# Kernel optimization log

Hardware: AMD Instinct MI355X
Metric: run time of the kernel (lower is better)

Reference implementation:

```python
import jax, jax.numpy as jnp
import numpy as np

N_EMBD = 768
N_HEAD = 12
HEAD_DIM = N_EMBD // N_HEAD
B, S = 2, 2048


def setup_inputs() -> dict:
    key = jax.random.key(0)
    k1, k2, k3 = jax.random.split(key, 3)
    scale = 0.02
    return {
        "hidden_states": jax.random.normal(k1, (B, S, N_EMBD), dtype=jnp.float32),
        "w_attn": jax.random.normal(k2, (N_EMBD, 3 * N_EMBD), dtype=jnp.float32) * scale,
        "b_attn": jnp.zeros((3 * N_EMBD,), dtype=jnp.float32),
        "w_proj": jax.random.normal(k3, (N_EMBD, N_EMBD), dtype=jnp.float32) * scale,
        "b_proj": jnp.zeros((N_EMBD,), dtype=jnp.float32),
    }


def reference(hidden_states, w_attn, b_attn, w_proj, b_proj):
    b, s, d = hidden_states.shape
    qkv = hidden_states @ w_attn + b_attn  # [B,S,3D]
    q, k, v = jnp.split(qkv, 3, axis=-1)
    # split heads: [B,S,D] -> [B,H,S,hd]
    def split_heads(t):
        return t.reshape(b, s, N_HEAD, HEAD_DIM).transpose(0, 2, 1, 3)
    q, k, v = split_heads(q), split_heads(k), split_heads(v)
    scores = jnp.einsum("bhqd,bhkd->bhqk", q, k) / jnp.sqrt(jnp.float32(HEAD_DIM))
    # causal mask: strict upper triangle -> -inf
    mask = jnp.triu(jnp.ones((s, s), dtype=bool), k=1)
    scores = jnp.where(mask, -jnp.inf, scores)
    attn = jax.nn.softmax(scores, axis=-1)
    out = jnp.einsum("bhqk,bhkd->bhqd", attn, v)  # [B,H,S,hd]
    out = out.transpose(0, 2, 1, 3).reshape(b, s, d)  # merge heads
    return out @ w_proj + b_proj
```

## Files before the change

### kernel.cpp

```cpp
#include <hip/hip_runtime.h>
#include <hip/hip_bf16.h>

#define BATCH 2
#define SEQ   2048
#define DMODEL 768
#define NHEAD 12
#define HDIM  64
#define QKVD  2304

typedef __bf16 bf16x8 __attribute__((ext_vector_type(8)));
typedef float f32x4 __attribute__((ext_vector_type(4)));
typedef float f32x16 __attribute__((ext_vector_type(16)));

static __device__ inline f32x4 mfma16(bf16x8 a, bf16x8 b, f32x4 c) {
    return __builtin_amdgcn_mfma_f32_16x16x32_bf16(a, b, c, 0, 0, 0);
}
static __device__ inline f32x16 mfma32(bf16x8 a, bf16x8 b, f32x16 c) {
    return __builtin_amdgcn_mfma_f32_32x32x16_bf16(a, b, c, 0, 0, 0);
}

static __device__ inline unsigned short f2bf_bits(float f) {
    __hip_bfloat16 h = __float2bfloat16(f);
    return __builtin_bit_cast(unsigned short, h);
}
static __device__ inline unsigned int pack_bf16(float a, float b) {
    return (unsigned int)f2bf_bits(a) | ((unsigned int)f2bf_bits(b) << 16);
}

static __device__ inline void gload16(const __hip_bfloat16* g, __hip_bfloat16* l) {
    __builtin_amdgcn_global_load_lds(
        (const __attribute__((address_space(1))) void*)g,
        (__attribute__((address_space(3))) void*)l, 16, 0, 0);
}


__global__ __launch_bounds__(256) void f32_to_bf16_k(const float* __restrict__ in,
                                                     __hip_bfloat16* __restrict__ out) {
    int i = blockIdx.x * 256 + threadIdx.x;
    float4 v = reinterpret_cast<const float4*>(in)[i];
    ushort4 o;
    o.x = f2bf_bits(v.x); o.y = f2bf_bits(v.y);
    o.z = f2bf_bits(v.z); o.w = f2bf_bits(v.w);
    reinterpret_cast<ushort4*>(out)[i] = o;
}

__global__ __launch_bounds__(256) void transpose_f32_to_bf16(const float* __restrict__ in,
                                                             __hip_bfloat16* __restrict__ out,
                                                             int R, int C) {
    __shared__ float t[32][33];
    int tx = threadIdx.x & 31, ty = threadIdx.x >> 5;
    int bx = blockIdx.x * 32;
    int by = blockIdx.y * 32;
#pragma unroll
    for (int k = 0; k < 4; k++)
        t[ty + k * 8][tx] = in[(size_t)(by + ty + k * 8) * C + bx + tx];
    __syncthreads();
#pragma unroll
    for (int k = 0; k < 4; k++)
        out[(size_t)(bx + ty + k * 8) * R + by + tx] = __float2bfloat16(t[tx][ty + k * 8]);
}


__global__ __launch_bounds__(256) void pack_kv(const __hip_bfloat16* __restrict__ qkv,
                                               __hip_bfloat16* __restrict__ Kp,
                                               __hip_bfloat16* __restrict__ Vp) {
    __shared__ __hip_bfloat16 Kl[32][72];
    __shared__ __hip_bfloat16 Vl[32][72];
    int tid = threadIdx.x;
    int q32 = blockIdx.x;
    int bh = blockIdx.y;
    int b = bh / NHEAD, h = bh - (bh / NHEAD) * NHEAD;
    int row = tid >> 3, cc = (tid & 7) * 8;
    const __hip_bfloat16* src = qkv + (size_t)(b * SEQ + q32 * 32 + row) * QKVD + h * HDIM + cc;
    *reinterpret_cast<uint4*>(&Kl[row][cc]) = *reinterpret_cast<const uint4*>(src + DMODEL);
    *reinterpret_cast<uint4*>(&Vl[row][cc]) = *reinterpret_cast<const uint4*>(src + 2 * DMODEL);
    __syncthreads();

    int l31 = tid & 31, half = (tid >> 5) & 1;
    size_t obase = (size_t)bh * 131072 + (size_t)q32 * 2048 + (size_t)tid * 8;

    int kd = tid >> 6;
    bf16x8 kf = *reinterpret_cast<const bf16x8*>(&Kl[l31][kd * 16 + half * 8]);
    *reinterpret_cast<bf16x8*>(Kp + obase) = kf;

    int ks = tid >> 7, dh = (tid >> 6) & 1;
    union { unsigned short s[8]; bf16x8 v; } vf;
#pragma unroll
    for (int i = 0; i < 8; i++)
        vf.s[i] = __builtin_bit_cast(unsigned short, Vl[ks * 16 + half * 8 + i][dh * 32 + l31]);
    *reinterpret_cast<bf16x8*>(Vp + obase) = vf.v;
}


template <bool OUT_BF16>
__global__ __launch_bounds__(256) void gemm_bt(const __hip_bfloat16* __restrict__ A,
                                               const __hip_bfloat16* __restrict__ Bt,
                                               const float* __restrict__ bias,
                                               void* __restrict__ Cp,
                                               int M, int N, int K, int lda) {
    __shared__ __hip_bfloat16 Al[2][128 * 32];
    __shared__ __hip_bfloat16 Bl[2][128 * 32];

    int tid = threadIdx.x;
    int wid = tid >> 6;
    int lane = tid & 63;
    int lr = lane & 15;
    int lg = lane >> 4;
    int m0 = blockIdx.y * 128;
    int n0 = blockIdx.x * 128;
    int wm = (wid >> 1) * 64;
    int wn = (wid & 1) * 64;

    int srow = wid * 16 + (lane >> 2);
    int scol = (lane & 3) * 8;
    const __hip_bfloat16* ag = A + (size_t)(m0 + srow) * lda + scol;
    const __hip_bfloat16* bg = Bt + (size_t)(n0 + srow) * K + scol;
    int lofs = wid * 512;

    f32x4 acc[4][4] = {};

    gload16(ag, &Al[0][lofs]);
    gload16(ag + (size_t)64 * lda, &Al[0][lofs + 2048]);
    gload16(bg, &Bl[0][lofs]);
    gload16(bg + (size_t)64 * K, &Bl[0][lofs + 2048]);
    __syncthreads();

    int nk = K >> 5;
    for (int t = 0; t < nk; t++) {
        int cb = t & 1;
        if (t + 1 < nk) {
            int k0 = (t + 1) << 5;
            int nb = cb ^ 1;
            gload16(ag + k0, &Al[nb][lofs]);
            gload16(ag + (size_t)64 * lda + k0, &Al[nb][lofs + 2048]);
            gload16(bg + k0, &Bl[nb][lofs]);
            gload16(bg + (size_t)64 * K + k0, &Bl[nb][lofs + 2048]);
        }

        bf16x8 af[4], bfr[4];
#pragma unroll
        for (int i = 0; i < 4; i++)
            af[i] = *reinterpret_cast<const bf16x8*>(&Al[cb][(wm + i * 16 + lr) * 32 + lg * 8]);
#pragma unroll
        for (int j = 0; j < 4; j++)
            bfr[j] = *reinterpret_cast<const bf16x8*>(&Bl[cb][(wn + j * 16 + lr) * 32 + lg * 8]);
#pragma unroll
        for (int i = 0; i < 4; i++)
#pragma unroll
            for (int j = 0; j < 4; j++)
                acc[i][j] = mfma16(af[i], bfr[j], acc[i][j]);
        __syncthreads();
    }

#pragma unroll
    for (int i = 0; i < 4; i++) {
#pragma unroll
        for (int j = 0; j < 4; j++) {
            int col = n0 + wn + j * 16 + lr;
            float bv = bias[col];
#pragma unroll
            for (int r = 0; r < 4; r++) {
                int row = m0 + wm + i * 16 + lg * 4 + r;
                float v = acc[i][j][r] + bv;
                if (OUT_BF16)
                    ((__hip_bfloat16*)Cp)[(size_t)row * N + col] = __float2bfloat16(v);
                else
                    ((float*)Cp)[(size_t)row * N + col] = v;
            }
        }
    }
}


#define KS2 0.18033688f

__global__ __launch_bounds__(256, 4) void flash_attn(const __hip_bfloat16* __restrict__ qkv,
                                                     const __hip_bfloat16* __restrict__ Kp,
                                                     const __hip_bfloat16* __restrict__ Vp,
                                                     __hip_bfloat16* __restrict__ obase) {
    __shared__ __align__(16) char smem[30208];

    int tid = threadIdx.x;
    int w = tid >> 6;
    int lane = tid & 63;
    int l31 = lane & 31;
    int lg2 = lane >> 5;

    int wg = blockIdx.x;
    int xcd = wg & 7;
    int slot = wg >> 3;
    int hsl = slot % 3;
    int qsl = slot / 3;
    int bh = xcd * 3 + hsl;
    int it = 63 - qsl;
    int b = bh / NHEAD;
    int h = bh - b * NHEAD;
    int q0 = it * 32;
    int bbase = b * SEQ;

    int Tw = (it >= w) ? ((it - w) >> 2) + 1 : 0;

    const __hip_bfloat16* Kph = Kp + (size_t)bh * 131072;
    const __hip_bfloat16* Vph = Vp + (size_t)bh * 131072;

    const __hip_bfloat16* qg = qkv + (size_t)(bbase + q0 + l31) * QKVD + h * HDIM;
    bf16x8 qf[4];
#pragma unroll
    for (int kd = 0; kd < 4; kd++)
        qf[kd] = *reinterpret_cast<const bf16x8*>(qg + kd * 16 + lg2 * 8);

    f32x16 o0 = {}, o1 = {};
    float m = -3.0e38f, l = 0.f;

    bf16x8 kc[4];
    {
        const __hip_bfloat16* kr = Kph + (size_t)w * 2048 + l31 * 8;
#pragma unroll
        for (int kd = 0; kd < 4; kd++)
            kc[kd] = *reinterpret_cast<const bf16x8*>(kr + (kd * 2 + lg2) * 256);
    }

    for (int t = 0; t < Tw; t++) {
        int qi = 4 * t + w;
        int kvbase = qi * 32;
        bool hn = (t + 1 < Tw);

        const __hip_bfloat16* vr = Vph + (size_t)qi * 2048 + lg2 * 256 + l31 * 8;
        bf16x8 vf[4];
#pragma unroll
        for (int ks = 0; ks < 2; ks++)
#pragma unroll
            for (int dh = 0; dh < 2; dh++)
                vf[ks * 2 + dh] = *reinterpret_cast<const bf16x8*>(vr + (ks * 2 + dh) * 512);

        __builtin_amdgcn_s_setprio(1);
        f32x16 st = {};
#pragma unroll
        for (int kd = 0; kd < 4; kd++)
            st = mfma32(kc[kd], qf[kd], st);
        __builtin_amdgcn_s_setprio(0);

        if (hn) {
            const __hip_bfloat16* kr = Kph + (size_t)(qi + 4) * 2048 + l31 * 8;
#pragma unroll
            for (int kd = 0; kd < 4; kd++)
                kc[kd] = *reinterpret_cast<const bf16x8*>(kr + (kd * 2 + lg2) * 256);
        }

        if (kvbase == q0) {
#pragma unroll
            for (int j = 0; j < 16; j++) {
                int kvl = (j & 3) + 8 * (j >> 2) + 4 * lg2;
                if (kvl > l31) st[j] = -3.0e38f;
            }
        }
        float tm[16];
#pragma unroll
        for (int j = 0; j < 16; j++) tm[j] = st[j];
#pragma unroll
        for (int dd = 8; dd >= 1; dd >>= 1)
#pragma unroll
            for (int j = 0; j < 8; j++)
                if (j < dd) tm[j] = fmaxf(tm[j], tm[j + dd]);
        float mx = fmaxf(tm[0], __shfl_xor(tm[0], 32, 64));
        bool small = __all(mx <= m + 44.0f);
        float mnew = small ? m : fmaxf(m, mx);
#pragma unroll
        for (int j = 0; j < 16; j++)
            st[j] = __builtin_amdgcn_exp2f((st[j] - mnew) * KS2);
        float ts[16];
#pragma unroll
        for (int j = 0; j < 16; j++) ts[j] = st[j];
#pragma unroll
        for (int dd = 8; dd >= 1; dd >>= 1)
#pragma unroll
            for (int j = 0; j < 8; j++)
                if (j < dd) ts[j] += ts[j + dd];
        float ls = ts[0] + __shfl_xor(ts[0], 32, 64);
        if (small) {
            l += ls;
        } else {
            float sc = __builtin_amdgcn_exp2f((m - mnew) * KS2);
            l = l * sc + ls;
            o0 *= sc;
            o1 *= sc;
            m = mnew;
        }

#pragma unroll
        for (int ks = 0; ks < 2; ks++) {
            unsigned int a0 = pack_bf16(st[8 * ks + 0], st[8 * ks + 1]);
            unsigned int a1 = pack_bf16(st[8 * ks + 2], st[8 * ks + 3]);
            unsigned int b0 = pack_bf16(st[8 * ks + 4], st[8 * ks + 5]);
            unsigned int b1 = pack_bf16(st[8 * ks + 6], st[8 * ks + 7]);
            unsigned int y0 = lg2 ? a0 : b0;
            unsigned int y1 = lg2 ? a1 : b1;
            unsigned int p0 = __shfl_xor(y0, 32, 64);
            unsigned int p1 = __shfl_xor(y1, 32, 64);
            union { unsigned int u[4]; bf16x8 v; } pf;
            pf.u[0] = lg2 ? p0 : a0;
            pf.u[1] = lg2 ? p1 : a1;
            pf.u[2] = lg2 ? b0 : p0;
            pf.u[3] = lg2 ? b1 : p1;
            __builtin_amdgcn_s_setprio(1);
            o0 = mfma32(vf[ks * 2 + 0], pf.v, o0);
            o1 = mfma32(vf[ks * 2 + 1], pf.v, o1);
            __builtin_amdgcn_s_setprio(0);
        }
    }

    __syncthreads();

    if (w != 0) {
        float* SCw = (float*)(smem + (w - 1) * 8448);
#pragma unroll
        for (int j = 0; j < 16; j++) {
            int dl = (j & 3) + 8 * (j >> 2) + 4 * lg2;
            SCw[dl * 32 + l31] = o0[j];
            SCw[(32 + dl) * 32 + l31] = o1[j];
        }
        if (lg2 == 0) {
            SCw[2048 + l31] = m;
            SCw[2048 + 32 + l31] = l;
        }
    }
    __syncthreads();
    if (w == 0) {
        float* SC1 = (float*)(smem + 0);
        float* SC2 = (float*)(smem + 8448);
        float* SC3 = (float*)(smem + 16896);
        __hip_bfloat16* OL = (__hip_bfloat16*)(smem + 25344);
        float m1 = SC1[2048 + l31], l1 = SC1[2048 + 32 + l31];
        float m2 = SC2[2048 + l31], l2 = SC2[2048 + 32 + l31];
        float m3 = SC3[2048 + l31], l3 = SC3[2048 + 32 + l31];
        float M = fmaxf(fmaxf(m, m1), fmaxf(m2, m3));
        float e0 = __builtin_amdgcn_exp2f((m - M) * KS2);
        float e1 = __builtin_amdgcn_exp2f((m1 - M) * KS2);
        float e2 = __builtin_amdgcn_exp2f((m2 - M) * KS2);
        float e3 = __builtin_amdgcn_exp2f((m3 - M) * KS2);
        float L = l * e0 + l1 * e1 + l2 * e2 + l3 * e3;
        float linv = 1.0f / L;
#pragma unroll
        for (int od = 0; od < 2; od++) {
#pragma unroll
            for (int g = 0; g < 4; g++) {
                int dbase = od * 32 + 8 * g + 4 * lg2;
                ushort4 w4;
#pragma unroll
                for (int r = 0; r < 4; r++) {
                    int d = dbase + r;
                    float self = od ? o1[4 * g + r] : o0[4 * g + r];
                    float v = self * e0 + SC1[d * 32 + l31] * e1 +
                              SC2[d * 32 + l31] * e2 + SC3[d * 32 + l31] * e3;
                    v *= linv;
                    ((unsigned short*)&w4)[r] = f2bf_bits(v);
                }
                *reinterpret_cast<ushort4*>(&OL[l31 * 72 + dbase]) = w4;
            }
        }
    }
    __syncthreads();
    {
        __hip_bfloat16* OL = (__hip_bfloat16*)(smem + 25344);
        int r = tid >> 3, c = (tid & 7) * 8;
        __hip_bfloat16* dst = obase + (size_t)(bbase + q0 + r) * QKVD + h * HDIM + c;
        *reinterpret_cast<uint4*>(dst) = *reinterpret_cast<const uint4*>(&OL[r * 72 + c]);
    }
}


extern "C" void kernel_launch(void* const* d_in, const int* in_sizes, int n_in,
                              void* d_out, int out_size, void* d_ws, size_t ws_size,
                              hipStream_t stream) {
    const float* hidden = (const float*)d_in[0];
    const float* w_attn = (const float*)d_in[1];
    const float* b_attn = (const float*)d_in[2];
    const float* w_proj = (const float*)d_in[3];
    const float* b_proj = (const float*)d_in[4];
    float* out = (float*)d_out;

    char* ws = (char*)d_ws;
    __hip_bfloat16* Xb  = (__hip_bfloat16*)(ws + 0);
    __hip_bfloat16* Wta = (__hip_bfloat16*)(ws + 6291456);
    __hip_bfloat16* Wtp = (__hip_bfloat16*)(ws + 9830400);
    __hip_bfloat16* QKV = (__hip_bfloat16*)(ws + 11010048);
    __hip_bfloat16* Kpb = (__hip_bfloat16*)(ws + 0);
    __hip_bfloat16* Vpb = (__hip_bfloat16*)(ws + 29884416);

    const int M = BATCH * SEQ;

    f32_to_bf16_k<<<dim3(M * DMODEL / (256 * 4)), dim3(256), 0, stream>>>(hidden, Xb);
    transpose_f32_to_bf16<<<dim3(QKVD / 32, DMODEL / 32), dim3(256), 0, stream>>>(w_attn, Wta, DMODEL, QKVD);
    transpose_f32_to_bf16<<<dim3(DMODEL / 32, DMODEL / 32), dim3(256), 0, stream>>>(w_proj, Wtp, DMODEL, DMODEL);
    gemm_bt<true><<<dim3(QKVD / 128, M / 128), dim3(256), 0, stream>>>(Xb, Wta, b_attn, QKV, M, QKVD, DMODEL, DMODEL);
    pack_kv<<<dim3(SEQ / 32, BATCH * NHEAD), dim3(256), 0, stream>>>(QKV, Kpb, Vpb);
    flash_attn<<<dim3(1536), dim3(256), 0, stream>>>(QKV, Kpb, Vpb, QKV + DMODEL);
    gemm_bt<false><<<dim3(DMODEL / 128, M / 128), dim3(256), 0, stream>>>(QKV + DMODEL, Wtp, b_proj, out, M, DMODEL, DMODEL, QKVD);
}
```

Baseline: 94.40 us.

## Fuse K/V packing into QKV GEMM epilogue and drop pack_kv kernel

```diff
diff --git a/kernel.cpp b/kernel.cpp
--- a/kernel.cpp
+++ b/kernel.cpp
@@ -61,34 +61,108 @@
 }
 
 
-__global__ __launch_bounds__(256) void pack_kv(const __hip_bfloat16* __restrict__ qkv,
-                                               __hip_bfloat16* __restrict__ Kp,
-                                               __hip_bfloat16* __restrict__ Vp) {
-    __shared__ __hip_bfloat16 Kl[32][72];
-    __shared__ __hip_bfloat16 Vl[32][72];
+__global__ __launch_bounds__(256) void gemm_qkv(const __hip_bfloat16* __restrict__ A,
+                                                const __hip_bfloat16* __restrict__ Bt,
+                                                const float* __restrict__ bias,
+                                                __hip_bfloat16* __restrict__ Qp,
+                                                __hip_bfloat16* __restrict__ Kp,
+                                                __hip_bfloat16* __restrict__ Vp,
+                                                int M, int N, int K) {
+    __shared__ __hip_bfloat16 Al[2][128 * 32];
+    __shared__ __hip_bfloat16 Bl[2][128 * 32];
+
     int tid = threadIdx.x;
-    int q32 = blockIdx.x;
-    int bh = blockIdx.y;
-    int b = bh / NHEAD, h = bh - (bh / NHEAD) * NHEAD;
-    int row = tid >> 3, cc = (tid & 7) * 8;
-    const __hip_bfloat16* src = qkv + (size_t)(b * SEQ + q32 * 32 + row) * QKVD + h * HDIM + cc;
-    *reinterpret_cast<uint4*>(&Kl[row][cc]) = *reinterpret_cast<const uint4*>(src + DMODEL);
-    *reinterpret_cast<uint4*>(&Vl[row][cc]) = *reinterpret_cast<const uint4*>(src + 2 * DMODEL);
-    __syncthreads();
-
-    int l31 = tid & 31, half = (tid >> 5) & 1;
-    size_t obase = (size_t)bh * 131072 + (size_t)q32 * 2048 + (size_t)tid * 8;
-
-    int kd = tid >> 6;
-    bf16x8 kf = *reinterpret_cast<const bf16x8*>(&Kl[l31][kd * 16 + half * 8]);
-    *reinterpret_cast<bf16x8*>(Kp + obase) = kf;
-
-    int ks = tid >> 7, dh = (tid >> 6) & 1;
-    union { unsigned short s[8]; bf16x8 v; } vf;
-#pragma unroll
-    for (int i = 0; i < 8; i++)
-        vf.s[i] = __builtin_bit_cast(unsigned short, Vl[ks * 16 + half * 8 + i][dh * 32 + l31]);
-    *reinterpret_cast<bf16x8*>(Vp + obase) = vf.v;
+    int wid = tid >> 6;
+    int lane = tid & 63;
+    int lr = lane & 15;
+    int lg = lane >> 4;
+    int m0 = blockIdx.y * 128;
+    int n0 = blockIdx.x * 128;
+    int wm = (wid >> 1) * 64;
+    int wn = (wid & 1) * 64;
+
+    int srow = wid * 16 + (lane >> 2);
+    int scol = (lane & 3) * 8;
+    const __hip_bfloat16* ag = A + (size_t)(m0 + srow) * K + scol;
+    const __hip_bfloat16* bg = Bt + (size_t)(n0 + srow) * K + scol;
+    int lofs = wid * 512;
+
+    f32x4 acc[4][4] = {};
+
+    gload16(ag, &Al[0][lofs]);
+    gload16(ag + (size_t)64 * K, &Al[0][lofs + 2048]);
+    gload16(bg, &Bl[0][lofs]);
+    gload16(bg + (size_t)64 * K, &Bl[0][lofs + 2048]);
+    __syncthreads();
+
+    int nk = K >> 5;
+    for (int t = 0; t < nk; t++) {
+        int cb = t & 1;
+        if (t + 1 < nk) {
+            int k0 = (t + 1) << 5;
+            int nb = cb ^ 1;
+            gload16(ag + k0, &Al[nb][lofs]);
+            gload16(ag + (size_t)64 * K + k0, &Al[nb][lofs + 2048]);
+            gload16(bg + k0, &Bl[nb][lofs]);
+            gload16(bg + (size_t)64 * K + k0, &Bl[nb][lofs + 2048]);
+        }
+
+        bf16x8 af[4], bfr[4];
+#pragma unroll
+        for (int i = 0; i < 4; i++)
+            af[i] = *reinterpret_cast<const bf16x8*>(&Al[cb][(wm + i * 16 + lr) * 32 + lg * 8]);
+#pragma unroll
+        for (int j = 0; j < 4; j++)
+            bfr[j] = *reinterpret_cast<const bf16x8*>(&Bl[cb][(wn + j * 16 + lr) * 32 + lg * 8]);
+#pragma unroll
+        for (int i = 0; i < 4; i++)
+#pragma unroll
+            for (int j = 0; j < 4; j++)
+                acc[i][j] = mfma16(af[i], bfr[j], acc[i][j]);
+        __syncthreads();
+    }
+
+#pragma unroll
+    for (int j = 0; j < 4; j++) {
+        int col = n0 + wn + j * 16 + lr;
+        float bv = bias[col];
+        int reg = col / DMODEL;
+        int cm = col - reg * DMODEL;
+        int h = cm >> 6;
+        int dd = cm & 63;
+        __hip_bfloat16* dstQK = (reg == 0) ? Qp : Kp;
+        if (reg < 2) {
+            int kd = dd >> 4, half = (dd >> 3) & 1, e = dd & 7;
+            int tbase = (kd * 2 + half) * 32;
+#pragma unroll
+            for (int i = 0; i < 4; i++) {
+#pragma unroll
+                for (int r = 0; r < 4; r++) {
+                    int row = m0 + wm + i * 16 + lg * 4 + r;
+                    int bq = row >> 11, tok = row & 2047;
+                    size_t off = (size_t)(bq * NHEAD + h) * 131072 + (size_t)(tok >> 5) * 2048
+                               + (size_t)(tbase + (tok & 31)) * 8 + e;
+                    dstQK[off] = __float2bfloat16(acc[i][j][r] + bv);
+                }
+            }
+        } else {
+            int dh = dd >> 5, l31v = dd & 31;
+#pragma unroll
+            for (int i = 0; i < 4; i++) {
+                int row0 = m0 + wm + i * 16 + lg * 4;
+                int bq = row0 >> 11, tok0 = row0 & 2047;
+                int ks = (tok0 >> 4) & 1, half = (tok0 >> 3) & 1;
+                size_t off = (size_t)(bq * NHEAD + h) * 131072 + (size_t)(tok0 >> 5) * 2048
+                           + (size_t)((((ks * 2 + dh) * 2 + half) * 32) + l31v) * 8 + (tok0 & 7);
+                ushort4 w4;
+                w4.x = f2bf_bits(acc[i][j][0] + bv);
+                w4.y = f2bf_bits(acc[i][j][1] + bv);
+                w4.z = f2bf_bits(acc[i][j][2] + bv);
+                w4.w = f2bf_bits(acc[i][j][3] + bv);
+                *reinterpret_cast<ushort4*>(Vp + off) = w4;
+            }
+        }
+    }
 }
 
 
@@ -174,10 +248,10 @@
 
 #define KS2 0.18033688f
 
-__global__ __launch_bounds__(256, 4) void flash_attn(const __hip_bfloat16* __restrict__ qkv,
+__global__ __launch_bounds__(256, 4) void flash_attn(const __hip_bfloat16* __restrict__ Qp,
                                                      const __hip_bfloat16* __restrict__ Kp,
                                                      const __hip_bfloat16* __restrict__ Vp,
-                                                     __hip_bfloat16* __restrict__ obase) {
+                                                     __hip_bfloat16* __restrict__ AO) {
     __shared__ __align__(16) char smem[30208];
 
     int tid = threadIdx.x;
@@ -203,11 +277,13 @@
     const __hip_bfloat16* Kph = Kp + (size_t)bh * 131072;
     const __hip_bfloat16* Vph = Vp + (size_t)bh * 131072;
 
-    const __hip_bfloat16* qg = qkv + (size_t)(bbase + q0 + l31) * QKVD + h * HDIM;
     bf16x8 qf[4];
-#pragma unroll
-    for (int kd = 0; kd < 4; kd++)
-        qf[kd] = *reinterpret_cast<const bf16x8*>(qg + kd * 16 + lg2 * 8);
+    {
+        const __hip_bfloat16* qr = Qp + (size_t)bh * 131072 + (size_t)it * 2048 + l31 * 8;
+#pragma unroll
+        for (int kd = 0; kd < 4; kd++)
+            qf[kd] = *reinterpret_cast<const bf16x8*>(qr + (kd * 2 + lg2) * 256);
+    }
 
     f32x16 o0 = {}, o1 = {};
     float m = -3.0e38f, l = 0.f;
@@ -363,7 +439,7 @@
     {
         __hip_bfloat16* OL = (__hip_bfloat16*)(smem + 25344);
         int r = tid >> 3, c = (tid & 7) * 8;
-        __hip_bfloat16* dst = obase + (size_t)(bbase + q0 + r) * QKVD + h * HDIM + c;
+        __hip_bfloat16* dst = AO + (size_t)(bbase + q0 + r) * DMODEL + h * HDIM + c;
         *reinterpret_cast<uint4*>(dst) = *reinterpret_cast<const uint4*>(&OL[r * 72 + c]);
     }
 }
@@ -383,17 +459,17 @@
     __hip_bfloat16* Xb  = (__hip_bfloat16*)(ws + 0);
     __hip_bfloat16* Wta = (__hip_bfloat16*)(ws + 6291456);
     __hip_bfloat16* Wtp = (__hip_bfloat16*)(ws + 9830400);
-    __hip_bfloat16* QKV = (__hip_bfloat16*)(ws + 11010048);
-    __hip_bfloat16* Kpb = (__hip_bfloat16*)(ws + 0);
-    __hip_bfloat16* Vpb = (__hip_bfloat16*)(ws + 29884416);
+    __hip_bfloat16* Qpb = (__hip_bfloat16*)(ws + 11010048);
+    __hip_bfloat16* Kpb = (__hip_bfloat16*)(ws + 17301504);
+    __hip_bfloat16* Vpb = (__hip_bfloat16*)(ws + 23592960);
+    __hip_bfloat16* AO  = (__hip_bfloat16*)(ws + 29884416);
 
     const int M = BATCH * SEQ;
 
     f32_to_bf16_k<<<dim3(M * DMODEL / (256 * 4)), dim3(256), 0, stream>>>(hidden, Xb);
     transpose_f32_to_bf16<<<dim3(QKVD / 32, DMODEL / 32), dim3(256), 0, stream>>>(w_attn, Wta, DMODEL, QKVD);
     transpose_f32_to_bf16<<<dim3(DMODEL / 32, DMODEL / 32), dim3(256), 0, stream>>>(w_proj, Wtp, DMODEL, DMODEL);
-    gemm_bt<true><<<dim3(QKVD / 128, M / 128), dim3(256), 0, stream>>>(Xb, Wta, b_attn, QKV, M, QKVD, DMODEL, DMODEL);
-    pack_kv<<<dim3(SEQ / 32, BATCH * NHEAD), dim3(256), 0, stream>>>(QKV, Kpb, Vpb);
-    flash_attn<<<dim3(1536), dim3(256), 0, stream>>>(QKV, Kpb, Vpb, QKV + DMODEL);
-    gemm_bt<false><<<dim3(DMODEL / 128, M / 128), dim3(256), 0, stream>>>(QKV + DMODEL, Wtp, b_proj, out, M, DMODEL, DMODEL, QKVD);
-}
+    gemm_qkv<<<dim3(QKVD / 128, M / 128), dim3(256), 0, stream>>>(Xb, Wta, b_attn, Qpb, Kpb, Vpb, M, QKVD, DMODEL);
+    flash_attn<<<dim3(1536), dim3(256), 0, stream>>>(Qpb, Kpb, Vpb, AO);
+    gemm_bt<false><<<dim3(DMODEL / 128, M / 128), dim3(256), 0, stream>>>(AO, Wtp, b_proj, out, M, DMODEL, DMODEL, DMODEL);
+}
```

Result: faster. 88.33 us (-6.4%).
